# Kernel optimization log

Measured on AMD Instinct MI355X. Metric: run time of the kernel, lower is better.

The kernel has to match this reference:

```python
import jax, jax.numpy as jnp
import numpy as np

B, N, C = 2, 65536, 256
HEADS, DIM_HEAD, SLICE_NUM = 8, 64, 64
INNER = HEADS * DIM_HEAD


def setup_inputs() -> dict:
    key = jax.random.key(0)
    ks = jax.random.split(key, 7)
    s_in = 1.0 / np.sqrt(C)
    s_dh = 1.0 / np.sqrt(DIM_HEAD)
    return {
        "x": jax.random.normal(ks[0], (B, N, C), dtype=jnp.float32),
        "Wx": jax.random.uniform(ks[1], (C, INNER), jnp.float32, -s_in, s_in),
        "bx": jax.random.uniform(ks[2], (INNER,), jnp.float32, -s_in, s_in),
        "Wfx": jax.random.uniform(ks[3], (C, INNER), jnp.float32, -s_in, s_in),
        "bfx": jax.random.uniform(ks[4], (INNER,), jnp.float32, -s_in, s_in),
        "Wslice": jax.random.uniform(ks[5], (DIM_HEAD, SLICE_NUM), jnp.float32, -s_dh, s_dh),
        "bslice": jax.random.uniform(ks[6], (SLICE_NUM,), jnp.float32, -s_dh, s_dh),
        "temperature": jnp.ones((1, HEADS, 1, 1), dtype=jnp.float32) * 0.5,
    }


def reference(x, Wx, bx, Wfx, bfx, Wslice, bslice, temperature):
    b, n, _ = x.shape
    # Linear projections, split heads: (B, N, H*D) -> (B, H, N, D)
    px = (x @ Wx + bx).reshape(b, n, HEADS, DIM_HEAD).transpose(0, 2, 1, 3)
    fx = (x @ Wfx + bfx).reshape(b, n, HEADS, DIM_HEAD).transpose(0, 2, 1, 3)
    # Project onto slices: (B, H, N, S)
    slice_proj = px @ Wslice + bslice
    # Temperature-scaled softmax over slices
    temp = jnp.clip(temperature, 0.5, 5.0)
    slice_weights = jax.nn.softmax(slice_proj / temp, axis=-1)
    # Normalize by per-slice mass over tokens, then aggregate
    slice_norm = slice_weights.sum(axis=2)  # (B, H, S)
    normed = slice_weights / (slice_norm[:, :, None, :] + 0.01)
    slice_tokens = jnp.einsum("bhns,bhnd->bhsd", normed, fx)
    return slice_tokens
```

## Files before the change

### kernel.cpp

```cpp
#include <hip/hip_runtime.h>
#include <hip/hip_bf16.h>


typedef __attribute__((ext_vector_type(8))) short short8;
typedef __attribute__((ext_vector_type(4))) short short4v;
typedef __attribute__((ext_vector_type(4))) float float4v;
typedef __attribute__((ext_vector_type(2))) unsigned int uint2v;

#define MP 36
#define XP 264

#define DPP_ADD(s, ctrl)                                                     \
    s += __int_as_float(__builtin_amdgcn_mov_dpp(__float_as_int(s), ctrl,    \
                                                 0xF, 0xF, true))

__device__ __forceinline__ unsigned short f2bf(float f) {
    union { float f; unsigned int u; } v; v.f = f;
    unsigned int r = (v.u + 0x7FFFu + ((v.u >> 16) & 1u)) >> 16;
    return (unsigned short)r;
}

__device__ __forceinline__ unsigned int pack2(float a, float b) {
    __hip_bfloat162 h = __float22bfloat162_rn(float2{a, b});
    union { __hip_bfloat162 h; unsigned int u; } cv; cv.h = h;
    return cv.u;
}

__global__ __launch_bounds__(256)
void msfe_prep4(const float* __restrict__ Wx, const float* __restrict__ bx,
                const float* __restrict__ Wfx,
                const float* __restrict__ Wslice, const float* __restrict__ bslice,
                unsigned short* __restrict__ WtF, float* __restrict__ bcv) {
    const int b = blockIdx.x, t = threadIdx.x;
    if (b < 256) {
        const int head = b >> 5, oct = b & 31;
        __shared__ float Wsl[64 * 65];
        __shared__ float WxS[8 * 64];
        __shared__ unsigned short stg[8 * 64];
        #pragma unroll
        for (int i = 0; i < 16; ++i) {
            int idx = i * 256 + t; int d = idx >> 6, s = idx & 63;
            Wsl[d * 65 + s] = Wslice[idx];
        }
        #pragma unroll
        for (int i = 0; i < 2; ++i) {
            int idx = i * 256 + t; int j = idx >> 6, d = idx & 63;
            WxS[j * 64 + d] = Wx[(long)(oct * 8 + j) * 512 + head * 64 + d];
        }
        __syncthreads();
        const int s = t & 63;
        #pragma unroll
        for (int rep = 0; rep < 2; ++rep) {
            int j = (t >> 6) + rep * 4;
            float a0 = 0.f, a1 = 0.f, a2 = 0.f, a3 = 0.f;
            #pragma unroll
            for (int d = 0; d < 64; d += 4) {
                a0 += WxS[j * 64 + d]     * Wsl[(d)     * 65 + s];
                a1 += WxS[j * 64 + d + 1] * Wsl[(d + 1) * 65 + s];
                a2 += WxS[j * 64 + d + 2] * Wsl[(d + 2) * 65 + s];
                a3 += WxS[j * 64 + d + 3] * Wsl[(d + 3) * 65 + s];
            }
            stg[j * 64 + s] = f2bf((a0 + a1) + (a2 + a3));
        }
        __syncthreads();
        if (t < 64) {
            int nt = t >> 4, l16 = t & 15;
            int ks = oct >> 2, quad = oct & 3;
            int lane = quad * 16 + l16;
            short8 o;
            #pragma unroll
            for (int j = 0; j < 8; ++j) o[j] = (short)stg[j * 64 + nt * 16 + l16];
            *(short8*)(WtF + ((((long)(0 * 8 + head) * 4 + nt) * 8 + ks) * 64 + lane) * 8) = o;
        }
    } else if (b < 320) {
        const int head = (b - 256) >> 3, ks = (b - 256) & 7;
        const int nt = t >> 6, lane = t & 63;
        const int quad = lane >> 4, l16 = lane & 15;
        short8 o;
        #pragma unroll
        for (int j = 0; j < 8; ++j)
            o[j] = (short)f2bf(Wfx[(long)(ks * 32 + quad * 8 + j) * 512 + head * 64 + nt * 16 + l16]);
        *(short8*)(WtF + ((((long)(1 * 8 + head) * 4 + nt) * 8 + ks) * 64 + lane) * 8) = o;
    } else {
        #pragma unroll
        for (int p = 0; p < 2; ++p) {
            int j = t + p * 256;
            int h = j >> 6, s = j & 63;
            float bsum = bslice[s];
            for (int d = 0; d < 64; ++d) bsum += bx[h * 64 + d] * Wslice[d * 64 + s];
            bcv[j] = bsum;
        }
    }
}

__global__ __launch_bounds__(256, 2)
void msfe_main10(const float* __restrict__ x,
                 const unsigned short* __restrict__ WtF,
                 const float* __restrict__ bcv,
                 const float* __restrict__ bfx,
                 const float* __restrict__ temperature,
                 float* __restrict__ Tg, float* __restrict__ ng) {
    __shared__ unsigned short wT[2][64 * MP];
    __shared__ unsigned short fT[2][64 * MP];
    __shared__ __align__(16) unsigned short XS[2][32 * XP];

    const int tid  = threadIdx.x;
    const int lane = tid & 63;
    const int wv   = tid >> 6;
    const int quad = lane >> 4;
    const int l16  = lane & 15;

    const int bidx = blockIdx.x;
    const int tile = (bidx >> 6) * 8 + (bidx & 7);
    const int head = (bidx >> 3) & 7;
    const int batch = tile >> 7;

    const int proj = wv >> 1;
    const int tw   = wv & 1;

    short8 wfr[4][8];
    {
        const unsigned short* wb = WtF + (((long)(proj * 8 + head) * 4) * 8) * 512 + (long)lane * 8;
        #pragma unroll
        for (int nt = 0; nt < 4; ++nt)
            #pragma unroll
            for (int ks = 0; ks < 8; ++ks)
                wfr[nt][ks] = *(const short8*)(wb + (nt * 8 + ks) * 512);
    }
    #pragma unroll
    for (int nt = 0; nt < 4; ++nt)
        #pragma unroll
        for (int ks = 0; ks < 8; ++ks)
            asm volatile("" : "+a"(wfr[nt][ks]));

    float tmp = temperature[head];
    tmp = fminf(fmaxf(tmp, 0.5f), 5.0f);
    const float invt = 1.0f / tmp;
    const float invt2 = invt * 1.44269504088896f;

    float bias[4];
    #pragma unroll
    for (int nt = 0; nt < 4; ++nt)
        bias[nt] = (proj == 0 ? bcv : bfx)[head * 64 + nt * 16 + l16];
    if (proj == 0) {
        #pragma unroll
        for (int nt = 0; nt < 4; ++nt) bias[nt] *= invt2;
    }

    float4v Tac[4];
    #pragma unroll
    for (int nt = 0; nt < 4; ++nt) Tac[nt] = (float4v){0.f, 0.f, 0.f, 0.f};
    float normAcc[4] = {0.f, 0.f, 0.f, 0.f};

    const float4v* xg4 = (const float4v*)(x + (long)tile * 512 * 256);

    {
        float4v xs[8];
        #pragma unroll
        for (int i = 0; i < 8; ++i) xs[i] = xg4[i * 256 + tid];
        #pragma unroll
        for (int i = 0; i < 8; ++i) {
            uint2v p;
            p.x = pack2(xs[i].x, xs[i].y);
            p.y = pack2(xs[i].z, xs[i].w);
            *(uint2v*)(&XS[0][(i * 4 + wv) * XP + lane * 4]) = p;
        }
    }
    __syncthreads();

    for (int c = 0; c < 16; ++c) {
        const int wbuf = c & 1, rbuf = wbuf ^ 1;

        short8 afr[8];
        #pragma unroll
        for (int ks = 0; ks < 8; ++ks)
            afr[ks] = *(const short8*)(&XS[wbuf][(tw * 16 + l16) * XP + ks * 32 + quad * 8]);

        float4v acc[4];
        #pragma unroll
        for (int nt = 0; nt < 4; ++nt) acc[nt] = (float4v){0.f, 0.f, 0.f, 0.f};
        __builtin_amdgcn_s_setprio(1);
        #pragma unroll
        for (int ks = 0; ks < 8; ++ks) {
            #pragma unroll
            for (int nt = 0; nt < 4; ++nt)
                acc[nt] = __builtin_amdgcn_mfma_f32_16x16x32_bf16(afr[ks], wfr[nt][ks], acc[nt], 0, 0, 0);
        }
        __builtin_amdgcn_s_setprio(0);

        float4v xst[8];
        if (c < 15) {
            #pragma unroll
            for (int i = 0; i < 8; ++i)
                xst[i] = xg4[(c + 1) * 2048 + i * 256 + tid];
        }

        if (c > 0) {
            short8 a = *(const short8*)(&wT[rbuf][(wv * 16 + l16) * MP + quad * 8]);
            __builtin_amdgcn_s_setprio(1);
            #pragma unroll
            for (int nt = 0; nt < 4; ++nt) {
                short8 bf = *(const short8*)(&fT[rbuf][(nt * 16 + l16) * MP + quad * 8]);
                Tac[nt] = __builtin_amdgcn_mfma_f32_16x16x32_bf16(a, bf, Tac[nt], 0, 0, 0);
            }
            __builtin_amdgcn_s_setprio(0);
        }

        if (proj == 0) {
            float e[4][4];
            #pragma unroll
            for (int nt = 0; nt < 4; ++nt)
                #pragma unroll
                for (int rr = 0; rr < 4; ++rr)
                    e[nt][rr] = exp2f(fmaf(acc[nt][rr], invt2, bias[nt]));
            #pragma unroll
            for (int rr = 0; rr < 4; ++rr) {
                float s = (e[0][rr] + e[1][rr]) + (e[2][rr] + e[3][rr]);
                DPP_ADD(s, 0x128);
                DPP_ADD(s, 0x124);
                DPP_ADD(s, 0x122);
                DPP_ADD(s, 0x121);
                float inv = __builtin_amdgcn_rcpf(s);
                e[0][rr] *= inv; e[1][rr] *= inv; e[2][rr] *= inv; e[3][rr] *= inv;
            }
            #pragma unroll
            for (int nt = 0; nt < 4; ++nt) {
                normAcc[nt] += e[nt][0] + e[nt][1] + e[nt][2] + e[nt][3];
                uint2v p;
                p.x = pack2(e[nt][0], e[nt][1]);
                p.y = pack2(e[nt][2], e[nt][3]);
                *(uint2v*)(&wT[wbuf][(nt * 16 + l16) * MP + tw * 16 + quad * 4]) = p;
            }
        } else {
            #pragma unroll
            for (int nt = 0; nt < 4; ++nt) {
                uint2v p;
                p.x = pack2(acc[nt][0] + bias[nt], acc[nt][1] + bias[nt]);
                p.y = pack2(acc[nt][2] + bias[nt], acc[nt][3] + bias[nt]);
                *(uint2v*)(&fT[wbuf][(nt * 16 + l16) * MP + tw * 16 + quad * 4]) = p;
            }
        }

        if (c < 15) {
            #pragma unroll
            for (int i = 0; i < 8; ++i) {
                uint2v p;
                p.x = pack2(xst[i].x, xst[i].y);
                p.y = pack2(xst[i].z, xst[i].w);
                *(uint2v*)(&XS[rbuf][(i * 4 + wv) * XP + lane * 4]) = p;
            }
        }

        __syncthreads();
    }

    {
        short8 a = *(const short8*)(&wT[1][(wv * 16 + l16) * MP + quad * 8]);
        #pragma unroll
        for (int nt = 0; nt < 4; ++nt) {
            short8 bf = *(const short8*)(&fT[1][(nt * 16 + l16) * MP + quad * 8]);
            Tac[nt] = __builtin_amdgcn_mfma_f32_16x16x32_bf16(a, bf, Tac[nt], 0, 0, 0);
        }
    }

    const int basehs = (batch * 8 + head) * 64;
    #pragma unroll
    for (int nt = 0; nt < 4; ++nt) {
        #pragma unroll
        for (int rr = 0; rr < 4; ++rr) {
            int s = wv * 16 + quad * 4 + rr;
            int d = nt * 16 + l16;
            atomicAdd(&Tg[(basehs + s) * 64 + d], Tac[nt][rr]);
        }
    }
    if (proj == 0) {
        #pragma unroll
        for (int nt = 0; nt < 4; ++nt) {
            float v = normAcc[nt];
            v += __shfl_xor(v, 16);
            v += __shfl_xor(v, 32);
            if (quad == 0) atomicAdd(&ng[basehs + nt * 16 + l16], v);
        }
    }
}

__global__ void msfe_final(const float* __restrict__ Tg, const float* __restrict__ ng,
                           float* __restrict__ out) {
    int i = blockIdx.x * 256 + threadIdx.x;
    out[i] = Tg[i] / (ng[i >> 6] + 0.01f);
}

extern "C" void kernel_launch(void* const* d_in, const int* in_sizes, int n_in,
                              void* d_out, int out_size, void* d_ws, size_t ws_size,
                              hipStream_t stream) {
    const float* x       = (const float*)d_in[0];
    const float* Wx      = (const float*)d_in[1];
    const float* bx      = (const float*)d_in[2];
    const float* Wfx     = (const float*)d_in[3];
    const float* bfx     = (const float*)d_in[4];
    const float* Wslice  = (const float*)d_in[5];
    const float* bslice  = (const float*)d_in[6];
    const float* temp    = (const float*)d_in[7];

    char* ws = (char*)d_ws;
    unsigned short* WtF = (unsigned short*)ws;
    float* bc = (float*)(ws + 524288);
    float* Tg = (float*)(ws + 526336);
    float* ng = (float*)(ws + 788480);

    hipMemsetAsync(Tg, 0, 262144 + 4096, stream);
    msfe_prep4<<<321, 256, 0, stream>>>(Wx, bx, Wfx, Wslice, bslice, WtF, bc);
    msfe_main10<<<2048, 256, 0, stream>>>(x, WtF, bc, bfx, temp, Tg, ng);
    msfe_final<<<256, 256, 0, stream>>>(Tg, ng, (float*)d_out);
}
```

Measured before the change: 309.1 us.

## Replace global atomic accumulation with per-tile partials and a reduction kernel

Each main-kernel block now writes its 64x64 slice-token partial and its per-slice norm partial to a private workspace slot instead of issuing float atomicAdds into shared accumulators. A new final kernel sums the 128 tile partials per batch-head, reduces the norm partials with shuffles, and divides. This removes the memset and the atomic contention, but it adds about 32 MB of partial writes and reads through global memory.

```diff
diff --git a/kernel.cpp b/kernel.cpp
--- a/kernel.cpp
+++ b/kernel.cpp
@@ -94,12 +94,12 @@
 }
 
 __global__ __launch_bounds__(256, 2)
-void msfe_main10(const float* __restrict__ x,
+void msfe_main11(const float* __restrict__ x,
                  const unsigned short* __restrict__ WtF,
                  const float* __restrict__ bcv,
                  const float* __restrict__ bfx,
                  const float* __restrict__ temperature,
-                 float* __restrict__ Tg, float* __restrict__ ng) {
+                 float* __restrict__ Pg, float* __restrict__ ngP) {
     __shared__ unsigned short wT[2][64 * MP];
     __shared__ unsigned short fT[2][64 * MP];
     __shared__ __align__(16) unsigned short XS[2][32 * XP];
@@ -263,14 +263,16 @@
         }
     }
 
-    const int basehs = (batch * 8 + head) * 64;
+    const int bh = batch * 8 + head;
+    const int tslot = tile & 127;
+    float* Pb = Pg + (long)(bh * 128 + tslot) * 4096;
     #pragma unroll
     for (int nt = 0; nt < 4; ++nt) {
         #pragma unroll
         for (int rr = 0; rr < 4; ++rr) {
             int s = wv * 16 + quad * 4 + rr;
             int d = nt * 16 + l16;
-            atomicAdd(&Tg[(basehs + s) * 64 + d], Tac[nt][rr]);
+            Pb[s * 64 + d] = Tac[nt][rr];
         }
     }
     if (proj == 0) {
@@ -279,15 +281,67 @@
             float v = normAcc[nt];
             v += __shfl_xor(v, 16);
             v += __shfl_xor(v, 32);
-            if (quad == 0) atomicAdd(&ng[basehs + nt * 16 + l16], v);
-        }
-    }
-}
-
-__global__ void msfe_final(const float* __restrict__ Tg, const float* __restrict__ ng,
-                           float* __restrict__ out) {
-    int i = blockIdx.x * 256 + threadIdx.x;
-    out[i] = Tg[i] / (ng[i >> 6] + 0.01f);
+            if (quad == 0)
+                ngP[((long)(bh * 128 + tslot) * 2 + wv) * 64 + nt * 16 + l16] = v;
+        }
+    }
+}
+
+__global__ __launch_bounds__(256)
+void msfe_final2(const float* __restrict__ Pg, const float* __restrict__ ngP,
+                 float* __restrict__ out) {
+    __shared__ float redp[4][4];
+    __shared__ float ngs[4];
+    __shared__ float4v red2[256];
+
+    const int tid = threadIdx.x;
+    const int bh = blockIdx.x >> 4;
+    const int s0 = (blockIdx.x & 15) * 4;
+
+    {
+        const float* gp = ngP + ((long)bh * 256 + tid) * 64 + s0;
+        float v0 = gp[0], v1 = gp[1], v2 = gp[2], v3 = gp[3];
+        #pragma unroll
+        for (int m = 1; m < 64; m <<= 1) {
+            v0 += __shfl_xor(v0, m); v1 += __shfl_xor(v1, m);
+            v2 += __shfl_xor(v2, m); v3 += __shfl_xor(v3, m);
+        }
+        if ((tid & 63) == 0) {
+            int w = tid >> 6;
+            redp[0][w] = v0; redp[1][w] = v1; redp[2][w] = v2; redp[3][w] = v3;
+        }
+        __syncthreads();
+        if (tid < 4)
+            ngs[tid] = ((redp[tid][0] + redp[tid][1]) + (redp[tid][2] + redp[tid][3])) + 0.01f;
+    }
+
+    const int d4 = tid & 15;
+    const int ss = (tid >> 4) & 3;
+    const int tq = tid >> 6;
+    const float4v* pp = (const float4v*)Pg;
+    const long base = (long)(bh * 128 + tq * 32) * 1024 + (s0 + ss) * 16 + d4;
+    float4v a4 = (float4v){0.f, 0.f, 0.f, 0.f};
+    #pragma unroll 8
+    for (int t = 0; t < 32; ++t) {
+        float4v v = pp[base + (long)t * 1024];
+        a4.x += v.x; a4.y += v.y; a4.z += v.z; a4.w += v.w;
+    }
+    red2[tid] = a4;
+    __syncthreads();
+    if (tid < 64) {
+        int ss2 = tid >> 4, dd4 = tid & 15;
+        float4v a = red2[0 * 64 + ss2 * 16 + dd4];
+        float4v b = red2[1 * 64 + ss2 * 16 + dd4];
+        float4v c = red2[2 * 64 + ss2 * 16 + dd4];
+        float4v d = red2[3 * 64 + ss2 * 16 + dd4];
+        float inv = 1.0f / ngs[ss2];
+        float4v o;
+        o.x = (a.x + b.x + c.x + d.x) * inv;
+        o.y = (a.y + b.y + c.y + d.y) * inv;
+        o.z = (a.z + b.z + c.z + d.z) * inv;
+        o.w = (a.w + b.w + c.w + d.w) * inv;
+        ((float4v*)out)[(long)bh * 1024 + (s0 + ss2) * 16 + dd4] = o;
+    }
 }
 
 extern "C" void kernel_launch(void* const* d_in, const int* in_sizes, int n_in,
@@ -303,13 +357,12 @@
     const float* temp    = (const float*)d_in[7];
 
     char* ws = (char*)d_ws;
-    unsigned short* WtF = (unsigned short*)ws;
-    float* bc = (float*)(ws + 524288);
-    float* Tg = (float*)(ws + 526336);
-    float* ng = (float*)(ws + 788480);
-
-    hipMemsetAsync(Tg, 0, 262144 + 4096, stream);
+    float* Pg  = (float*)ws;
+    float* ngP = (float*)(ws + 33554432);
+    unsigned short* WtF = (unsigned short*)(ws + 34603008);
+    float* bc  = (float*)(ws + 35127296);
+
     msfe_prep4<<<321, 256, 0, stream>>>(Wx, bx, Wfx, Wslice, bslice, WtF, bc);
-    msfe_main10<<<2048, 256, 0, stream>>>(x, WtF, bc, bfx, temp, Tg, ng);
-    msfe_final<<<256, 256, 0, stream>>>(Tg, ng, (float*)d_out);
-}
+    msfe_main11<<<2048, 256, 0, stream>>>(x, WtF, bc, bfx, temp, Pg, ngP);
+    msfe_final2<<<256, 256, 0, stream>>>(Pg, ngP, (float*)d_out);
+}
```

Measured after the change: 314.1 us. Within noise of the previous version (+1.6%).
